# Optimization experiments

Hardware: AMD Instinct MI355X
Metric: run time of the kernel (lower is better)

Reference implementation:

```python
import jax, jax.numpy as jnp
import numpy as np

BETA = 0.25

def setup_inputs() -> dict:
    key = jax.random.key(0)
    k1, k2 = jax.random.split(key)
    z = jax.random.normal(k1, (32, 64, 64, 64), dtype=jnp.float32)  # (B, D, H, W)
    # EmbeddingEMA init: uniform(-1/K, 1/K)
    K, D = 1024, 64
    weight = jax.random.uniform(k2, (K, D), dtype=jnp.float32, minval=-1.0 / K, maxval=1.0 / K)
    return {"z": z, "weight": weight}


def reference(z, weight):
    b, d, h, w = z.shape
    K = weight.shape[0]
    # permute (B,D,H,W) -> (B,H,W,D) and flatten to (N, D)
    z_flat = jnp.transpose(z, (0, 2, 3, 1)).reshape(-1, d)
    # squared euclidean distance: ||z||^2 + ||c||^2 - 2 z c^T  -> (N, K)
    distance = (
        jnp.sum(z_flat * z_flat, axis=1, keepdims=True)
        + jnp.sum(weight * weight, axis=1)
        - 2.0 * jnp.matmul(z_flat, weight.T)
    )
    vq_indices = jnp.argmin(distance, axis=1)  # (N,)
    z_quantized = weight[vq_indices]  # gather (N, D)
    # one-hot scatter stats (training-time EMA inputs)
    vq_current_count = jax.ops.segment_sum(
        jnp.ones((z_flat.shape[0],), dtype=z_flat.dtype), vq_indices, num_segments=K)
    vq_current_sum = jax.ops.segment_sum(z_flat, vq_indices, num_segments=K)  # (K, D)
    commitment_loss = jnp.mean((z_flat - jax.lax.stop_gradient(z_quantized)) ** 2)
    loss = BETA * commitment_loss
    # straight-through estimator
    q = z_flat + jax.lax.stop_gradient(z_quantized - z_flat)
    q = jnp.transpose(q.reshape(b, h, w, d), (0, 3, 1, 2))  # back to (B, D, H, W)
    return q, loss, commitment_loss, vq_current_count, vq_current_sum
```

## Files before the change

kernel.cpp:

```cpp
#include <hip/hip_runtime.h>


#define HWsz   4096
#define Dd     64
#define Kk     1024
#define NB     32
#define NTOT   131072
#define QSIZE  (NTOT * Dd)
#define BETA_C 0.25f

typedef float  f32x4  __attribute__((ext_vector_type(4)));
typedef short  bf16x8 __attribute__((ext_vector_type(8)));

__device__ __forceinline__ unsigned short f2bf(float f) {
    unsigned u = __float_as_uint(f);
    u += 0x7FFF + ((u >> 16) & 1);
    return (unsigned short)(u >> 16);
}
__device__ __forceinline__ float bf2f(unsigned short b) {
    return __uint_as_float(((unsigned)b) << 16);
}

__global__ __launch_bounds__(256) void vq_prep(const float* __restrict__ w,
                                               float* __restrict__ c2,
                                               unsigned short* __restrict__ whi,
                                               unsigned short* __restrict__ wlo) {
    int t = blockIdx.x * 256 + threadIdx.x;
    int k = t >> 6, d = t & 63;
    float v = w[t];
    unsigned short hb = f2bf(v);
    unsigned short lb = f2bf(v - bf2f(hb));
    int ctile = k >> 4, col = k & 15;
    int s = d >> 5, kg = (d >> 3) & 3, j = d & 7;
    int idx = (((ctile * 2 + s) * 64) + kg * 16 + col) * 8 + j;
    whi[idx] = hb; wlo[idx] = lb;

    if (t < Kk) {
        const float4* c4 = reinterpret_cast<const float4*>(w + t * Dd);
        float s0 = 0.f, s1 = 0.f, s2 = 0.f, s3 = 0.f;
#pragma unroll
        for (int q = 0; q < 16; ++q) {
            float4 cq = c4[q];
            s0 = fmaf(cq.x, cq.x, s0); s1 = fmaf(cq.y, cq.y, s1);
            s2 = fmaf(cq.z, cq.z, s2); s3 = fmaf(cq.w, cq.w, s3);
        }
        c2[t] = (s0 + s1) + (s2 + s3);
    }
}

__global__ __launch_bounds__(256) void vq_dist(const float* __restrict__ z,
                                               const float* __restrict__ w,
                                               const float* __restrict__ c2,
                                               const unsigned short* __restrict__ whi,
                                               const unsigned short* __restrict__ wlo,
                                               float* __restrict__ out,
                                               float* __restrict__ accum,
                                               int* __restrict__ idx_ws) {
    const int lane = threadIdx.x & 63;
    const int wid  = threadIdx.x >> 6;
    const int b    = blockIdx.x >> 4;
    const int t0   = (blockIdx.x & 15) * 16 + wid * 4;
    const int col  = lane & 15;
    const int kg   = lane >> 4;

    bf16x8 zhi[4][2], zlo[4][2];
#pragma unroll
    for (int m = 0; m < 4; ++m) {
        const int hw0 = (t0 + m) << 4;
        const float* zbase = z + (size_t)b * (Dd * HWsz) + hw0 + col;
#pragma unroll
        for (int s = 0; s < 2; ++s) {
            bf16x8 h, l;
#pragma unroll
            for (int j = 0; j < 8; ++j) {
                float zz = zbase[(size_t)(32 * s + kg * 8 + j) * HWsz];
                unsigned short hb = f2bf(zz);
                unsigned short lb = f2bf(zz - bf2f(hb));
                h[j] = (short)hb; l[j] = (short)lb;
            }
            zhi[m][s] = h; zlo[m][s] = l;
        }
    }

    float best[4][4];
    int   bk[4][4];
#pragma unroll
    for (int m = 0; m < 4; ++m)
#pragma unroll
        for (int r = 0; r < 4; ++r) { best[m][r] = 3.4e38f; bk[m][r] = 0; }

    const bf16x8* ph = reinterpret_cast<const bf16x8*>(whi);
    const bf16x8* pl = reinterpret_cast<const bf16x8*>(wlo);

    for (int ct = 0; ct < 64; ++ct) {
        bf16x8 wh0 = ph[(ct * 2 + 0) * 64 + lane];
        bf16x8 wh1 = ph[(ct * 2 + 1) * 64 + lane];
        bf16x8 wl0 = pl[(ct * 2 + 0) * 64 + lane];
        bf16x8 wl1 = pl[(ct * 2 + 1) * 64 + lane];

        float cv = c2[ct * 16 + col];
        int   kc = ct * 16 + col;

#pragma unroll
        for (int m = 0; m < 4; ++m) {
            f32x4 za = {0.f, 0.f, 0.f, 0.f};
            f32x4 zb = {0.f, 0.f, 0.f, 0.f};
            za = __builtin_amdgcn_mfma_f32_16x16x32_bf16(zhi[m][0], wh0, za, 0, 0, 0);
            za = __builtin_amdgcn_mfma_f32_16x16x32_bf16(zhi[m][1], wh1, za, 0, 0, 0);
            za = __builtin_amdgcn_mfma_f32_16x16x32_bf16(zhi[m][0], wl0, za, 0, 0, 0);
            za = __builtin_amdgcn_mfma_f32_16x16x32_bf16(zhi[m][1], wl1, za, 0, 0, 0);
            zb = __builtin_amdgcn_mfma_f32_16x16x32_bf16(zlo[m][0], wh0, zb, 0, 0, 0);
            zb = __builtin_amdgcn_mfma_f32_16x16x32_bf16(zlo[m][1], wh1, zb, 0, 0, 0);
#pragma unroll
            for (int r = 0; r < 4; ++r) {
                float s = fmaf(-2.f, za[r] + zb[r], cv);
                if (s < best[m][r]) { best[m][r] = s; bk[m][r] = kc; }
            }
        }
    }

#pragma unroll
    for (int off = 1; off < 16; off <<= 1) {
#pragma unroll
        for (int m = 0; m < 4; ++m)
#pragma unroll
            for (int r = 0; r < 4; ++r) {
                float ob = __shfl_xor(best[m][r], off, 64);
                int   ok = __shfl_xor(bk[m][r],   off, 64);
                if (ob < best[m][r] || (ob == best[m][r] && ok < bk[m][r])) {
                    best[m][r] = ob; bk[m][r] = ok;
                }
            }
    }

    float commit = 0.f;
    const int srcl = (col >> 2) << 4;
    const int rsel = col & 3;
#pragma unroll
    for (int m = 0; m < 4; ++m) {
        int c0 = __shfl(bk[m][0], srcl, 64);
        int c1 = __shfl(bk[m][1], srcl, 64);
        int c2r = __shfl(bk[m][2], srcl, 64);
        int c3 = __shfl(bk[m][3], srcl, 64);
        int mybk = (rsel == 0) ? c0 : (rsel == 1) ? c1 : (rsel == 2) ? c2r : c3;

        const int hw0 = (t0 + m) << 4;
        if (lane < 16) idx_ws[(size_t)b * HWsz + hw0 + col] = mybk;

        float* qbase = out + (size_t)b * (Dd * HWsz) + hw0 + col;
#pragma unroll
        for (int s = 0; s < 2; ++s) {
            const float4* cw = reinterpret_cast<const float4*>(w + mybk * Dd + 32 * s + kg * 8);
            float4 p0 = cw[0], p1 = cw[1];
            float cb[8] = {p0.x, p0.y, p0.z, p0.w, p1.x, p1.y, p1.z, p1.w};
#pragma unroll
            for (int j = 0; j < 8; ++j) {
                int   d  = 32 * s + kg * 8 + j;
                float zz = bf2f((unsigned short)zhi[m][s][j]) +
                           bf2f((unsigned short)zlo[m][s][j]);
                float cc = cb[j];
                qbase[(size_t)d * HWsz] = zz + (cc - zz);
                float dd = zz - cc;
                commit = fmaf(dd, dd, commit);
            }
        }
    }

#pragma unroll
    for (int off = 32; off > 0; off >>= 1) commit += __shfl_down(commit, off, 64);

    __shared__ float red[4];
    if (lane == 0) red[wid] = commit;
    __syncthreads();
    if (threadIdx.x == 0)
        atomicAdd(accum, (red[0] + red[1]) + (red[2] + red[3]));
}

__global__ __launch_bounds__(256) void vq_stats(const float* __restrict__ z,
                                                const int* __restrict__ idx_ws,
                                                float* __restrict__ psum,
                                                float* __restrict__ pcnt) {
    const int b     = blockIdx.x >> 3;
    const int chunk = blockIdx.x & 7;
    const int dbase = chunk * 8;
    const bool docnt = (chunk == 0);

    __shared__ float acc[8][Kk];
    __shared__ float cnt[Kk];
    for (int i = threadIdx.x; i < 8 * Kk; i += 256)
        acc[i >> 10][i & 1023] = 0.f;
    for (int i = threadIdx.x; i < Kk; i += 256) cnt[i] = 0.f;
    __syncthreads();

    const int4* ip = reinterpret_cast<const int4*>(idx_ws + (size_t)b * HWsz);
#pragma unroll
    for (int it = 0; it < 4; ++it) {
        int c4 = it * 256 + threadIdx.x;
        int4 k4 = ip[c4];
#pragma unroll
        for (int d8 = 0; d8 < 8; ++d8) {
            const float4 v4 = reinterpret_cast<const float4*>(
                z + ((size_t)b * Dd + dbase + d8) * HWsz)[c4];
            atomicAdd(&acc[d8][k4.x], v4.x);
            atomicAdd(&acc[d8][k4.y], v4.y);
            atomicAdd(&acc[d8][k4.z], v4.z);
            atomicAdd(&acc[d8][k4.w], v4.w);
        }
        if (docnt) {
            atomicAdd(&cnt[k4.x], 1.f);
            atomicAdd(&cnt[k4.y], 1.f);
            atomicAdd(&cnt[k4.z], 1.f);
            atomicAdd(&cnt[k4.w], 1.f);
        }
    }
    __syncthreads();

    float* po = psum + (size_t)b * (Dd * Kk) + (size_t)dbase * Kk;
    for (int i = threadIdx.x; i < 8 * Kk; i += 256)
        po[i] = acc[i >> 10][i & 1023];
    if (docnt) {
        float* pc = pcnt + (size_t)b * Kk;
        for (int i = threadIdx.x; i < Kk; i += 256) pc[i] = cnt[i];
    }
}

__global__ __launch_bounds__(256) void vq_reduce(const float* __restrict__ psum,
                                                 const float* __restrict__ pcnt,
                                                 const float* __restrict__ accum,
                                                 float* __restrict__ out) {
    int t = blockIdx.x * 256 + threadIdx.x;
    int k = t & 1023, d = t >> 10;
    float s = 0.f;
#pragma unroll
    for (int b = 0; b < NB; ++b)
        s += psum[(size_t)b * (Dd * Kk) + (size_t)d * Kk + k];
    out[QSIZE + 2 + Kk + (size_t)k * Dd + d] = s;
    if (t < Kk) {
        float c = 0.f;
#pragma unroll
        for (int b = 0; b < NB; ++b) c += pcnt[((size_t)b << 10) + t];
        out[QSIZE + 2 + t] = c;
    }
    if (t == 0) {
        float c = accum[0] / (float)QSIZE;
        out[QSIZE]     = BETA_C * c;
        out[QSIZE + 1] = c;
    }
}

extern "C" void kernel_launch(void* const* d_in, const int* in_sizes, int n_in,
                              void* d_out, int out_size, void* d_ws, size_t ws_size,
                              hipStream_t stream) {
    const float* z = (const float*)d_in[0];
    const float* w = (const float*)d_in[1];
    float* out = (float*)d_out;

    float* accum = (float*)d_ws;
    float* c2    = (float*)d_ws + 64;
    unsigned short* whi = (unsigned short*)((float*)d_ws + 64 + Kk);
    unsigned short* wlo = whi + (Kk * Dd);
    int*   idx_ws = (int*)(wlo + (Kk * Dd));
    float* psum   = (float*)(idx_ws + NTOT);
    float* pcnt   = psum + (size_t)NB * Dd * Kk;

    hipMemsetAsync(accum, 0, 64 * sizeof(float), stream);

    vq_prep<<<(Kk * Dd) / 256, 256, 0, stream>>>(w, c2, whi, wlo);
    vq_dist<<<NTOT / 256, 256, 0, stream>>>(z, w, c2, whi, wlo, out, accum, idx_ws);
    vq_stats<<<NB * 8, 256, 0, stream>>>(z, idx_ws, psum, pcnt);
    vq_reduce<<<(Kk * Dd) / 256, 256, 0, stream>>>(psum, pcnt, accum, out);
}
```

Before: 243.0 us.

## Increase grid parallelism in distance and stats kernels, prefetch codebook, drop atomics

The distance kernel now gives each wave 2 row tiles instead of 4, which doubles the block count to 1024. It adds a launch-bounds occupancy hint and software-prefetches the next codebook tile's bf16 fragments and norms. The MFMA order is interleaved across two accumulators. The stats kernel splits each batch's positions into 4 slices, giving 4x more blocks at the cost of more partial sums for the reduce kernel. The commitment loss is now written per block and reduced in the final kernel rather than with a global atomic plus memset. Each wave reuses codebook loads less, and the reduce step reads more memory.

```diff
diff --git a/kernel.cpp b/kernel.cpp
--- a/kernel.cpp
+++ b/kernel.cpp
@@ -8,6 +8,7 @@
 #define NTOT   131072
 #define QSIZE  (NTOT * Dd)
 #define BETA_C 0.25f
+#define DIST_BLOCKS 1024
 
 typedef float  f32x4  __attribute__((ext_vector_type(4)));
 typedef short  bf16x8 __attribute__((ext_vector_type(8)));
@@ -48,24 +49,24 @@
     }
 }
 
-__global__ __launch_bounds__(256) void vq_dist(const float* __restrict__ z,
-                                               const float* __restrict__ w,
-                                               const float* __restrict__ c2,
-                                               const unsigned short* __restrict__ whi,
-                                               const unsigned short* __restrict__ wlo,
-                                               float* __restrict__ out,
-                                               float* __restrict__ accum,
-                                               int* __restrict__ idx_ws) {
+__global__ __launch_bounds__(256, 4) void vq_dist(const float* __restrict__ z,
+                                                  const float* __restrict__ w,
+                                                  const float* __restrict__ c2,
+                                                  const unsigned short* __restrict__ whi,
+                                                  const unsigned short* __restrict__ wlo,
+                                                  float* __restrict__ out,
+                                                  float* __restrict__ commit_ws,
+                                                  int* __restrict__ idx_ws) {
     const int lane = threadIdx.x & 63;
     const int wid  = threadIdx.x >> 6;
-    const int b    = blockIdx.x >> 4;
-    const int t0   = (blockIdx.x & 15) * 16 + wid * 4;
+    const int b    = blockIdx.x >> 5;
+    const int t0   = (blockIdx.x & 31) * 8 + wid * 2;
     const int col  = lane & 15;
     const int kg   = lane >> 4;
 
-    bf16x8 zhi[4][2], zlo[4][2];
-#pragma unroll
-    for (int m = 0; m < 4; ++m) {
+    bf16x8 zhi[2][2], zlo[2][2];
+#pragma unroll
+    for (int m = 0; m < 2; ++m) {
         const int hw0 = (t0 + m) << 4;
         const float* zbase = z + (size_t)b * (Dd * HWsz) + hw0 + col;
 #pragma unroll
@@ -82,47 +83,53 @@
         }
     }
 
-    float best[4][4];
-    int   bk[4][4];
-#pragma unroll
-    for (int m = 0; m < 4; ++m)
+    float best[2][4];
+    int   bk[2][4];
+#pragma unroll
+    for (int m = 0; m < 2; ++m)
 #pragma unroll
         for (int r = 0; r < 4; ++r) { best[m][r] = 3.4e38f; bk[m][r] = 0; }
 
     const bf16x8* ph = reinterpret_cast<const bf16x8*>(whi);
     const bf16x8* pl = reinterpret_cast<const bf16x8*>(wlo);
 
+    bf16x8 h0 = ph[lane], h1 = ph[64 + lane];
+    bf16x8 l0 = pl[lane], l1 = pl[64 + lane];
+    float  cv = c2[col];
+
+#pragma unroll 2
     for (int ct = 0; ct < 64; ++ct) {
-        bf16x8 wh0 = ph[(ct * 2 + 0) * 64 + lane];
-        bf16x8 wh1 = ph[(ct * 2 + 1) * 64 + lane];
-        bf16x8 wl0 = pl[(ct * 2 + 0) * 64 + lane];
-        bf16x8 wl1 = pl[(ct * 2 + 1) * 64 + lane];
-
-        float cv = c2[ct * 16 + col];
-        int   kc = ct * 16 + col;
-
-#pragma unroll
-        for (int m = 0; m < 4; ++m) {
+        const int nx = (ct + 1) & 63;
+        bf16x8 nh0 = ph[(nx * 2 + 0) * 64 + lane];
+        bf16x8 nh1 = ph[(nx * 2 + 1) * 64 + lane];
+        bf16x8 nl0 = pl[(nx * 2 + 0) * 64 + lane];
+        bf16x8 nl1 = pl[(nx * 2 + 1) * 64 + lane];
+        float  ncv = c2[nx * 16 + col];
+
+        const int kc = ct * 16 + col;
+#pragma unroll
+        for (int m = 0; m < 2; ++m) {
             f32x4 za = {0.f, 0.f, 0.f, 0.f};
             f32x4 zb = {0.f, 0.f, 0.f, 0.f};
-            za = __builtin_amdgcn_mfma_f32_16x16x32_bf16(zhi[m][0], wh0, za, 0, 0, 0);
-            za = __builtin_amdgcn_mfma_f32_16x16x32_bf16(zhi[m][1], wh1, za, 0, 0, 0);
-            za = __builtin_amdgcn_mfma_f32_16x16x32_bf16(zhi[m][0], wl0, za, 0, 0, 0);
-            za = __builtin_amdgcn_mfma_f32_16x16x32_bf16(zhi[m][1], wl1, za, 0, 0, 0);
-            zb = __builtin_amdgcn_mfma_f32_16x16x32_bf16(zlo[m][0], wh0, zb, 0, 0, 0);
-            zb = __builtin_amdgcn_mfma_f32_16x16x32_bf16(zlo[m][1], wh1, zb, 0, 0, 0);
+            za = __builtin_amdgcn_mfma_f32_16x16x32_bf16(zhi[m][0], h0, za, 0, 0, 0);
+            zb = __builtin_amdgcn_mfma_f32_16x16x32_bf16(zlo[m][0], h0, zb, 0, 0, 0);
+            za = __builtin_amdgcn_mfma_f32_16x16x32_bf16(zhi[m][1], h1, za, 0, 0, 0);
+            zb = __builtin_amdgcn_mfma_f32_16x16x32_bf16(zlo[m][1], h1, zb, 0, 0, 0);
+            za = __builtin_amdgcn_mfma_f32_16x16x32_bf16(zhi[m][0], l0, za, 0, 0, 0);
+            zb = __builtin_amdgcn_mfma_f32_16x16x32_bf16(zhi[m][1], l1, zb, 0, 0, 0);
 #pragma unroll
             for (int r = 0; r < 4; ++r) {
                 float s = fmaf(-2.f, za[r] + zb[r], cv);
                 if (s < best[m][r]) { best[m][r] = s; bk[m][r] = kc; }
             }
         }
+        h0 = nh0; h1 = nh1; l0 = nl0; l1 = nl1; cv = ncv;
     }
 
 #pragma unroll
     for (int off = 1; off < 16; off <<= 1) {
 #pragma unroll
-        for (int m = 0; m < 4; ++m)
+        for (int m = 0; m < 2; ++m)
 #pragma unroll
             for (int r = 0; r < 4; ++r) {
                 float ob = __shfl_xor(best[m][r], off, 64);
@@ -137,7 +144,7 @@
     const int srcl = (col >> 2) << 4;
     const int rsel = col & 3;
 #pragma unroll
-    for (int m = 0; m < 4; ++m) {
+    for (int m = 0; m < 2; ++m) {
         int c0 = __shfl(bk[m][0], srcl, 64);
         int c1 = __shfl(bk[m][1], srcl, 64);
         int c2r = __shfl(bk[m][2], srcl, 64);
@@ -173,29 +180,31 @@
     if (lane == 0) red[wid] = commit;
     __syncthreads();
     if (threadIdx.x == 0)
-        atomicAdd(accum, (red[0] + red[1]) + (red[2] + red[3]));
+        commit_ws[blockIdx.x] = (red[0] + red[1]) + (red[2] + red[3]);
 }
 
 __global__ __launch_bounds__(256) void vq_stats(const float* __restrict__ z,
                                                 const int* __restrict__ idx_ws,
                                                 float* __restrict__ psum,
-                                                float* __restrict__ pcnt) {
-    const int b     = blockIdx.x >> 3;
-    const int chunk = blockIdx.x & 7;
+                                                float* __restrict__ pcnt,
+                                                int nq) {
+    const int q     = blockIdx.x % nq;
+    const int tmp   = blockIdx.x / nq;
+    const int chunk = tmp & 7;
+    const int b     = tmp >> 3;
     const int dbase = chunk * 8;
     const bool docnt = (chunk == 0);
 
     __shared__ float acc[8][Kk];
     __shared__ float cnt[Kk];
-    for (int i = threadIdx.x; i < 8 * Kk; i += 256)
-        acc[i >> 10][i & 1023] = 0.f;
+    for (int i = threadIdx.x; i < 8 * Kk; i += 256) acc[i >> 10][i & 1023] = 0.f;
     for (int i = threadIdx.x; i < Kk; i += 256) cnt[i] = 0.f;
     __syncthreads();
 
+    const int pos4 = (HWsz / 4) / nq;
     const int4* ip = reinterpret_cast<const int4*>(idx_ws + (size_t)b * HWsz);
-#pragma unroll
-    for (int it = 0; it < 4; ++it) {
-        int c4 = it * 256 + threadIdx.x;
+    for (int c = threadIdx.x; c < pos4; c += 256) {
+        const int c4 = q * pos4 + c;
         int4 k4 = ip[c4];
 #pragma unroll
         for (int d8 = 0; d8 < 8; ++d8) {
@@ -215,36 +224,45 @@
     }
     __syncthreads();
 
-    float* po = psum + (size_t)b * (Dd * Kk) + (size_t)dbase * Kk;
-    for (int i = threadIdx.x; i < 8 * Kk; i += 256)
-        po[i] = acc[i >> 10][i & 1023];
+    float* po = psum + ((size_t)(b * nq + q) * Dd + dbase) * Kk;
+    for (int i = threadIdx.x; i < 8 * Kk; i += 256) po[i] = acc[i >> 10][i & 1023];
     if (docnt) {
-        float* pc = pcnt + (size_t)b * Kk;
+        float* pc = pcnt + (size_t)(b * nq + q) * Kk;
         for (int i = threadIdx.x; i < Kk; i += 256) pc[i] = cnt[i];
     }
 }
 
 __global__ __launch_bounds__(256) void vq_reduce(const float* __restrict__ psum,
                                                  const float* __restrict__ pcnt,
-                                                 const float* __restrict__ accum,
-                                                 float* __restrict__ out) {
+                                                 const float* __restrict__ commit_ws,
+                                                 float* __restrict__ out,
+                                                 int nparts) {
     int t = blockIdx.x * 256 + threadIdx.x;
     int k = t & 1023, d = t >> 10;
     float s = 0.f;
-#pragma unroll
-    for (int b = 0; b < NB; ++b)
-        s += psum[(size_t)b * (Dd * Kk) + (size_t)d * Kk + k];
+    for (int p = 0; p < nparts; ++p)
+        s += psum[((size_t)p * Dd + d) * Kk + k];
     out[QSIZE + 2 + Kk + (size_t)k * Dd + d] = s;
     if (t < Kk) {
         float c = 0.f;
-#pragma unroll
-        for (int b = 0; b < NB; ++b) c += pcnt[((size_t)b << 10) + t];
+        for (int p = 0; p < nparts; ++p) c += pcnt[(size_t)p * Kk + t];
         out[QSIZE + 2 + t] = c;
     }
-    if (t == 0) {
-        float c = accum[0] / (float)QSIZE;
-        out[QSIZE]     = BETA_C * c;
-        out[QSIZE + 1] = c;
+
+    if (blockIdx.x == 0) {
+        float cs = 0.f;
+        for (int i = threadIdx.x; i < DIST_BLOCKS; i += 256) cs += commit_ws[i];
+#pragma unroll
+        for (int off = 32; off > 0; off >>= 1) cs += __shfl_down(cs, off, 64);
+        __shared__ float r2[4];
+        const int lane = threadIdx.x & 63, wid = threadIdx.x >> 6;
+        if (lane == 0) r2[wid] = cs;
+        __syncthreads();
+        if (threadIdx.x == 0) {
+            float c = ((r2[0] + r2[1]) + (r2[2] + r2[3])) / (float)QSIZE;
+            out[QSIZE]     = BETA_C * c;
+            out[QSIZE + 1] = c;
+        }
     }
 }
 
@@ -255,18 +273,21 @@
     const float* w = (const float*)d_in[1];
     float* out = (float*)d_out;
 
-    float* accum = (float*)d_ws;
-    float* c2    = (float*)d_ws + 64;
-    unsigned short* whi = (unsigned short*)((float*)d_ws + 64 + Kk);
+    float* commit_ws = (float*)d_ws;
+    float* c2        = (float*)d_ws + 1024;
+    unsigned short* whi = (unsigned short*)((float*)d_ws + 2048);
     unsigned short* wlo = whi + (Kk * Dd);
     int*   idx_ws = (int*)(wlo + (Kk * Dd));
-    float* psum   = (float*)(idx_ws + NTOT);
-    float* pcnt   = psum + (size_t)NB * Dd * Kk;
-
-    hipMemsetAsync(accum, 0, 64 * sizeof(float), stream);
+    float* pcnt   = (float*)(idx_ws + NTOT);
+
+    size_t fixed_floats = 2048 + 65536 + 131072;
+    int nq = 4;
+    size_t need4 = (fixed_floats + (size_t)NB * 4 * Kk + (size_t)NB * 4 * Dd * Kk) * 4;
+    if (ws_size < need4) nq = 1;
+    float* psum = pcnt + (size_t)NB * nq * Kk;
 
     vq_prep<<<(Kk * Dd) / 256, 256, 0, stream>>>(w, c2, whi, wlo);
-    vq_dist<<<NTOT / 256, 256, 0, stream>>>(z, w, c2, whi, wlo, out, accum, idx_ws);
-    vq_stats<<<NB * 8, 256, 0, stream>>>(z, idx_ws, psum, pcnt);
-    vq_reduce<<<(Kk * Dd) / 256, 256, 0, stream>>>(psum, pcnt, accum, out);
-}
+    vq_dist<<<DIST_BLOCKS, 256, 0, stream>>>(z, w, c2, whi, wlo, out, commit_ws, idx_ws);
+    vq_stats<<<NB * 8 * nq, 256, 0, stream>>>(z, idx_ws, psum, pcnt, nq);
+    vq_reduce<<<(Kk * Dd) / 256, 256, 0, stream>>>(psum, pcnt, commit_ws, out, NB * nq);
+}
```

New measurement: 281.8 us. +16.0%, slower.
